# Kernel optimization log

Measured on AMD Instinct MI355X. Metric: run time of the kernel, lower is better.

Reference implementation:

```python
import jax, jax.numpy as jnp
import numpy as np

B, S, E, H = 2, 2048, 1024, 16
D = E // H  # head_dim = 64


def setup_inputs() -> dict:
    key = jax.random.key(0)
    ks = jax.random.split(key, 6)
    sc = 1.0 / np.sqrt(D)
    return {
        "x": jax.random.normal(ks[0], (B, S, E), dtype=jnp.float32),
        "Wq": jax.random.normal(ks[1], (D, D), dtype=jnp.float32) * sc,
        "Wk": jax.random.normal(ks[2], (D, D), dtype=jnp.float32) * sc,
        "Wv": jax.random.normal(ks[3], (D, D), dtype=jnp.float32) * sc,
        "Wo": jax.random.normal(ks[4], (E, E), dtype=jnp.float32) * (1.0 / np.sqrt(E)),
        "bo": jnp.zeros((E,), dtype=jnp.float32),
    }


def reference(x, Wq, Wk, Wv, Wo, bo):
    b, s, e = x.shape
    # split into heads: (B, H, S, D)
    xh = x.reshape(b, s, H, D).transpose(0, 2, 1, 3)
    # per-head linear projections (weights SHARED across heads); torch Linear: x @ W^T
    q = jnp.einsum('bhsd,ed->bhse', xh, Wq)
    k = jnp.einsum('bhsd,ed->bhse', xh, Wk)
    v = jnp.einsum('bhsd,ed->bhse', xh, Wv)
    # full attention matrix (B, H, S, S) — faithful to the naive original
    energy = jnp.einsum('bhqd,bhkd->bhqk', q, k)
    attn = jax.nn.softmax(energy / jnp.sqrt(jnp.asarray(D, x.dtype)), axis=-1)
    out = jnp.einsum('bhqk,bhkd->bhqd', attn, v)
    out = out.transpose(0, 2, 1, 3).reshape(b, s, e)
    return out @ Wo.T + bo
```

## Files before the change

### kernel.cpp

```cpp
#include <hip/hip_runtime.h>
#include <hip/hip_bf16.h>

#define B 2
#define S 2048
#define E 1024
#define H 16
#define D 64

typedef unsigned short ushort_t;
typedef __attribute__((ext_vector_type(8))) short bf16x8;
typedef __attribute__((ext_vector_type(4))) float f32x4;
typedef __attribute__((ext_vector_type(16))) float f32x16;

static __device__ __forceinline__ ushort_t f2bf(float f) {
    union { float f; unsigned u; } v; v.f = f;
    unsigned r = v.u + 0x7fffu + ((v.u >> 16) & 1u);
    return (ushort_t)(r >> 16);
}

#define MFMA(a, b, c)   __builtin_amdgcn_mfma_f32_16x16x32_bf16((a), (b), (c), 0, 0, 0)
#define MFMA32(a, b, c) __builtin_amdgcn_mfma_f32_32x32x16_bf16((a), (b), (c), 0, 0, 0)
#define PACKBF(hi, lo) __builtin_amdgcn_perm((hi), (lo), 0x07060302u)

__global__ __launch_bounds__(256) void cvt_w(
    const float* __restrict__ Wq, const float* __restrict__ Wk, const float* __restrict__ Wv,
    const float* __restrict__ Wo,
    ushort_t* __restrict__ wqb, ushort_t* __restrict__ wkb, ushort_t* __restrict__ wvb,
    ushort_t* __restrict__ wob)
{
    int gid = blockIdx.x, t = threadIdx.x;
    if (gid < 1024) {
        int i = gid * 1024 + t * 4;
        float4 f = *(const float4*)(Wo + i);
        ushort4 u; u.x = f2bf(f.x); u.y = f2bf(f.y); u.z = f2bf(f.z); u.w = f2bf(f.w);
        *(ushort4*)(wob + i) = u;
    } else {
        int idx = (gid - 1024) * 1024 + t * 4;
        int which = idx >> 12, off = idx & 4095;
        const float* src = (which == 0) ? Wq : (which == 1) ? Wk : Wv;
        ushort_t* dst    = (which == 0) ? wqb : (which == 1) ? wkb : wvb;
        float sc = (which == 0) ? 0.18033688011112042f : 1.0f;
        float4 f = *(const float4*)(src + off);
        ushort4 u; u.x = f2bf(f.x * sc); u.y = f2bf(f.y * sc);
        u.z = f2bf(f.z * sc); u.w = f2bf(f.w * sc);
        *(ushort4*)(dst + off) = u;
    }
}

__global__ __launch_bounds__(256) void qkv_proj(
    const float* __restrict__ x,
    const ushort_t* __restrict__ wq, const ushort_t* __restrict__ wk, const ushort_t* __restrict__ wv,
    ushort_t* __restrict__ q, ushort_t* __restrict__ k, ushort_t* __restrict__ vT)
{
    __shared__ ushort_t Xs[64][72];
    __shared__ ushort_t Wqs[64][72], Wks[64][72], Wvs[64][72];
    int t = threadIdx.x;
    int bh = blockIdx.y, b = bh >> 4, h = bh & 15;
    int s0 = blockIdx.x * 64;

    {
        int i = t >> 2, d0 = (t & 3) * 16;
        const float* xp = x + ((size_t)(b * S + s0 + i)) * E + h * D + d0;
        #pragma unroll
        for (int c = 0; c < 16; c += 4) {
            float4 f = *(const float4*)(xp + c);
            Xs[i][d0 + c + 0] = f2bf(f.x); Xs[i][d0 + c + 1] = f2bf(f.y);
            Xs[i][d0 + c + 2] = f2bf(f.z); Xs[i][d0 + c + 3] = f2bf(f.w);
        }
    }
    {
        int e = t >> 2, d0 = (t & 3) * 16;
        *(bf16x8*)&Wqs[e][d0]     = *(const bf16x8*)(wq + e * 64 + d0);
        *(bf16x8*)&Wqs[e][d0 + 8] = *(const bf16x8*)(wq + e * 64 + d0 + 8);
        *(bf16x8*)&Wks[e][d0]     = *(const bf16x8*)(wk + e * 64 + d0);
        *(bf16x8*)&Wks[e][d0 + 8] = *(const bf16x8*)(wk + e * 64 + d0 + 8);
        *(bf16x8*)&Wvs[e][d0]     = *(const bf16x8*)(wv + e * 64 + d0);
        *(bf16x8*)&Wvs[e][d0 + 8] = *(const bf16x8*)(wv + e * 64 + d0 + 8);
    }
    __syncthreads();

    int w = t >> 6, lane = t & 63, m = lane & 15, quad = lane >> 4;
    bf16x8 a0 = *(bf16x8*)&Xs[16 * w + m][quad * 8];
    bf16x8 a1 = *(bf16x8*)&Xs[16 * w + m][32 + quad * 8];
    f32x4 cq[4], ck[4], cv[4];
    #pragma unroll
    for (int nt = 0; nt < 4; nt++) { cq[nt] = (f32x4)0.f; ck[nt] = (f32x4)0.f; cv[nt] = (f32x4)0.f; }
    #pragma unroll
    for (int nt = 0; nt < 4; nt++) {
        bf16x8 b0, b1;
        b0 = *(bf16x8*)&Wqs[nt * 16 + m][quad * 8]; b1 = *(bf16x8*)&Wqs[nt * 16 + m][32 + quad * 8];
        cq[nt] = MFMA(a0, b0, cq[nt]); cq[nt] = MFMA(a1, b1, cq[nt]);
        b0 = *(bf16x8*)&Wks[nt * 16 + m][quad * 8]; b1 = *(bf16x8*)&Wks[nt * 16 + m][32 + quad * 8];
        ck[nt] = MFMA(a0, b0, ck[nt]); ck[nt] = MFMA(a1, b1, ck[nt]);
        b0 = *(bf16x8*)&Wvs[nt * 16 + m][quad * 8]; b1 = *(bf16x8*)&Wvs[nt * 16 + m][32 + quad * 8];
        cv[nt] = MFMA(a0, b0, cv[nt]); cv[nt] = MFMA(a1, b1, cv[nt]);
    }
    size_t base = (size_t)bh * S + s0;
    #pragma unroll
    for (int nt = 0; nt < 4; nt++)
        #pragma unroll
        for (int r = 0; r < 4; r++) {
            size_t idx = (base + 16 * w + quad * 4 + r) * D + nt * 16 + m;
            q[idx] = f2bf(cq[nt][r]);
            k[idx] = f2bf(ck[nt][r]);
        }
    __syncthreads();
    #pragma unroll
    for (int nt = 0; nt < 4; nt++)
        #pragma unroll
        for (int r = 0; r < 4; r++)
            Wvs[nt * 16 + m][16 * w + quad * 4 + r] = f2bf(cv[nt][r]);
    __syncthreads();
    {
        int d0 = t >> 2, sc = (t & 3) * 16;
        ushort_t* vp = vT + ((size_t)bh * D + d0) * S + s0 + sc;
        *(bf16x8*)(vp)     = *(bf16x8*)&Wvs[d0][sc];
        *(bf16x8*)(vp + 8) = *(bf16x8*)&Wvs[d0][sc + 8];
    }
}

__global__ __launch_bounds__(256) void flash_attn(
    const ushort_t* __restrict__ q, const ushort_t* __restrict__ k,
    const ushort_t* __restrict__ vT, ushort_t* __restrict__ ao)
{
    __shared__ ushort_t Ks[2][64][72];
    __shared__ ushort_t Vt[2][64][72];
    int t = threadIdx.x;
    int bh = blockIdx.y, b = bh >> 4, h = bh & 15;
    int q0 = blockIdx.x * 128;
    int w = t >> 6, lane = t & 63, l31 = lane & 31, half = lane >> 5;

    const ushort_t* qb = q + ((size_t)bh * S + q0) * D;
    const ushort_t* kb = k + (size_t)bh * S * D;
    const ushort_t* vb = vT + (size_t)bh * D * S;

    bf16x8 qf[4];
    {
        const ushort_t* qp = qb + (size_t)(w * 32 + l31) * D + half * 8;
        #pragma unroll
        for (int c = 0; c < 4; c++) qf[c] = *(const bf16x8*)(qp + c * 16);
    }

    f32x16 o0 = (f32x16)0.f, o1 = (f32x16)0.f;
    float2 ls2 = make_float2(0.f, 0.f);

    int sr = t >> 2, scc = (t & 3) * 16;
    bf16x8 kp0, kp1, vp0, vp1;

    {
        const ushort_t* kp = kb + (size_t)sr * D + scc;
        const ushort_t* vp = vb + (size_t)sr * S + scc;
        kp0 = *(const bf16x8*)(kp);     kp1 = *(const bf16x8*)(kp + 8);
        vp0 = *(const bf16x8*)(vp);     vp1 = *(const bf16x8*)(vp + 8);
        *(bf16x8*)&Ks[0][sr][scc]     = kp0;
        *(bf16x8*)&Ks[0][sr][scc + 8] = kp1;
        *(bf16x8*)&Vt[0][sr][scc]     = vp0;
        *(bf16x8*)&Vt[0][sr][scc + 8] = vp1;
    }
    __syncthreads();
    {
        const ushort_t* kp = kb + (size_t)(64 + sr) * D + scc;
        const ushort_t* vp = vb + (size_t)sr * S + 64 + scc;
        kp0 = *(const bf16x8*)(kp);     kp1 = *(const bf16x8*)(kp + 8);
        vp0 = *(const bf16x8*)(vp);     vp1 = *(const bf16x8*)(vp + 8);
    }

    const int NT = S / 64;
    for (int it = 0; it < NT; it++) {
        int p = it & 1;
        if (it + 1 < NT) {
            *(bf16x8*)&Ks[1 - p][sr][scc]     = kp0;
            *(bf16x8*)&Ks[1 - p][sr][scc + 8] = kp1;
            *(bf16x8*)&Vt[1 - p][sr][scc]     = vp0;
            *(bf16x8*)&Vt[1 - p][sr][scc + 8] = vp1;
        }
        if (it + 2 < NT) {
            int k0n = (it + 2) * 64;
            const ushort_t* kp = kb + (size_t)(k0n + sr) * D + scc;
            const ushort_t* vp = vb + (size_t)sr * S + k0n + scc;
            kp0 = *(const bf16x8*)(kp);     kp1 = *(const bf16x8*)(kp + 8);
            vp0 = *(const bf16x8*)(vp);     vp1 = *(const bf16x8*)(vp + 8);
        }

        union { unsigned u[4]; bf16x8 v; } pa[4];
        #pragma unroll
        for (int st = 0; st < 2; st++) {
            f32x16 e = (f32x16)0.f;
            #pragma unroll
            for (int c = 0; c < 4; c++) {
                bf16x8 ka = *(bf16x8*)&Ks[p][st * 32 + l31][c * 16 + half * 8];
                e = MFMA32(ka, qf[c], e);
            }
            unsigned pt[16];
            #pragma unroll
            for (int r = 0; r < 16; r += 2) {
                float pe0 = __builtin_amdgcn_exp2f(e[r]);
                float pe1 = __builtin_amdgcn_exp2f(e[r + 1]);
                ls2.x += pe0; ls2.y += pe1;
                pt[r]     = __float_as_uint(pe0);
                pt[r + 1] = __float_as_uint(pe1);
            }
            #pragma unroll
            for (int c2 = 0; c2 < 2; c2++) {
                int rb = c2 * 8;
                unsigned dA = PACKBF(pt[rb + 1], pt[rb + 0]);
                unsigned dB = PACKBF(pt[rb + 3], pt[rb + 2]);
                unsigned dC = PACKBF(pt[rb + 5], pt[rb + 4]);
                unsigned dD = PACKBF(pt[rb + 7], pt[rb + 6]);
                unsigned x1 = (unsigned)__shfl_xor((int)(half ? dA : dC), 32, 64);
                unsigned x2 = (unsigned)__shfl_xor((int)(half ? dB : dD), 32, 64);
                int kc = st * 2 + c2;
                pa[kc].u[0] = half ? x1 : dA;
                pa[kc].u[1] = half ? x2 : dB;
                pa[kc].u[2] = half ? dC : x1;
                pa[kc].u[3] = half ? dD : x2;
            }
        }

        #pragma unroll
        for (int kc = 0; kc < 4; kc++) {
            bf16x8 vf0 = *(bf16x8*)&Vt[p][l31][kc * 16 + half * 8];
            bf16x8 vf1 = *(bf16x8*)&Vt[p][32 + l31][kc * 16 + half * 8];
            o0 = MFMA32(pa[kc].v, vf0, o0);
            o1 = MFMA32(pa[kc].v, vf1, o1);
        }
        __syncthreads();
    }

    float lsum = ls2.x + ls2.y;
    float lfull = lsum + __shfl_xor(lsum, 32, 64);
    float inv = 1.001953125f / lfull;
    #pragma unroll
    for (int reg = 0; reg < 16; reg++) {
        int qrow = (reg & 3) + 8 * (reg >> 2) + 4 * half;
        float li = __shfl(inv, qrow, 64);
        int srow = q0 + w * 32 + qrow;
        size_t base = ((size_t)(b * S + srow)) * E + h * D + l31;
        ao[base]      = f2bf(o0[reg] * li);
        ao[base + 32] = f2bf(o1[reg] * li);
    }
}

__global__ __launch_bounds__(256) void out_proj(
    const ushort_t* __restrict__ A, const ushort_t* __restrict__ Wob,
    const float* __restrict__ bo, float* __restrict__ Y)
{
    __shared__ ushort_t As[2][128][72];
    __shared__ ushort_t Ws[2][64][72];
    int t = threadIdx.x;
    int n0 = blockIdx.x * 64, m0 = blockIdx.y * 128;
    int w = t >> 6, lane = t & 63, m = lane & 15, quad = lane >> 4;
    f32x4 acc[2][4];
    #pragma unroll
    for (int u = 0; u < 2; u++)
        #pragma unroll
        for (int nt = 0; nt < 4; nt++) acc[u][nt] = (f32x4)0.f;

    int ar = t >> 1, ac = (t & 1) * 32;
    int wr = t >> 2, wc = (t & 3) * 16;
    const ushort_t* apb = A + (size_t)(m0 + ar) * E + ac;
    const ushort_t* wpb = Wob + (size_t)(n0 + wr) * E + wc;

    bf16x8 arg[4], wrg[2];
    {
        #pragma unroll
        for (int i = 0; i < 4; i++) *(bf16x8*)&As[0][ar][ac + 8 * i] = *(const bf16x8*)(apb + 8 * i);
        *(bf16x8*)&Ws[0][wr][wc]     = *(const bf16x8*)(wpb);
        *(bf16x8*)&Ws[0][wr][wc + 8] = *(const bf16x8*)(wpb + 8);
    }
    __syncthreads();
    {
        #pragma unroll
        for (int i = 0; i < 4; i++) arg[i] = *(const bf16x8*)(apb + 64 + 8 * i);
        wrg[0] = *(const bf16x8*)(wpb + 64);
        wrg[1] = *(const bf16x8*)(wpb + 64 + 8);
    }

    const int KT = E / 64;
    for (int ks = 0; ks < KT; ks++) {
        int p = ks & 1;
        if (ks + 1 < KT) {
            #pragma unroll
            for (int i = 0; i < 4; i++) *(bf16x8*)&As[1 - p][ar][ac + 8 * i] = arg[i];
            *(bf16x8*)&Ws[1 - p][wr][wc]     = wrg[0];
            *(bf16x8*)&Ws[1 - p][wr][wc + 8] = wrg[1];
        }
        if (ks + 2 < KT) {
            int off = (ks + 2) * 64;
            #pragma unroll
            for (int i = 0; i < 4; i++) arg[i] = *(const bf16x8*)(apb + off + 8 * i);
            wrg[0] = *(const bf16x8*)(wpb + off);
            wrg[1] = *(const bf16x8*)(wpb + off + 8);
        }
        #pragma unroll
        for (int h2 = 0; h2 < 2; h2++) {
            bf16x8 af[2];
            af[0] = *(bf16x8*)&As[p][w * 32 + m][h2 * 32 + quad * 8];
            af[1] = *(bf16x8*)&As[p][w * 32 + 16 + m][h2 * 32 + quad * 8];
            #pragma unroll
            for (int nt = 0; nt < 4; nt++) {
                bf16x8 bfr = *(bf16x8*)&Ws[p][nt * 16 + m][h2 * 32 + quad * 8];
                acc[0][nt] = MFMA(af[0], bfr, acc[0][nt]);
                acc[1][nt] = MFMA(af[1], bfr, acc[1][nt]);
            }
        }
        __syncthreads();
    }
    #pragma unroll
    for (int u = 0; u < 2; u++)
        #pragma unroll
        for (int nt = 0; nt < 4; nt++)
            #pragma unroll
            for (int r = 0; r < 4; r++) {
                int row = m0 + w * 32 + u * 16 + quad * 4 + r;
                int col = n0 + nt * 16 + m;
                Y[(size_t)row * E + col] = acc[u][nt][r] + bo[col];
            }
}

extern "C" void kernel_launch(void* const* d_in, const int* in_sizes, int n_in,
                              void* d_out, int out_size, void* d_ws, size_t ws_size,
                              hipStream_t stream)
{
    const float* x  = (const float*)d_in[0];
    const float* Wq = (const float*)d_in[1];
    const float* Wk = (const float*)d_in[2];
    const float* Wv = (const float*)d_in[3];
    const float* Wo = (const float*)d_in[4];
    const float* bo = (const float*)d_in[5];
    float* Y = (float*)d_out;

    const size_t n = (size_t)B * H * S * D;
    ushort_t* qw  = (ushort_t*)d_ws;
    ushort_t* kw  = qw + n;
    ushort_t* vTw = kw + n;
    ushort_t* ao  = vTw + n;
    ushort_t* wob = ao + n;
    ushort_t* wqb = wob + (size_t)E * E;
    ushort_t* wkb = wqb + D * D;
    ushort_t* wvb = wkb + D * D;

    cvt_w<<<dim3(1024 + 12), 256, 0, stream>>>(Wq, Wk, Wv, Wo, wqb, wkb, wvb, wob);
    qkv_proj<<<dim3(S / 64, B * H), 256, 0, stream>>>(x, wqb, wkb, wvb, qw, kw, vTw);
    flash_attn<<<dim3(S / 128, B * H), 256, 0, stream>>>(qw, kw, vTw, ao);
    out_proj<<<dim3(E / 64, (B * S) / 128), 256, 0, stream>>>(ao, wob, bo, Y);
}
```

Baseline: 152.2 us.

## Fuse weight conversion into consumers and double per-warp query rows in attention

Drops the separate weight-conversion kernel: Q/K/V weights are now converted to bf16 inside qkv_proj, and Wo is converted on the fly inside out_proj's load pipeline. This removes one launch and a round trip of the converted weights through global memory. qkv_proj swaps MFMA operands so Q/K results can be stored as vectorized ushort4 rows instead of scalar stores. flash_attn moves to 128 threads with each warp handling two 32-row query groups, so each K fragment is reused twice. In exchange there are more registers per thread and fewer waves per block, and out_proj repeats the Wo fp32 conversion once per row tile.

```diff
diff --git a/kernel.cpp b/kernel.cpp
--- a/kernel.cpp
+++ b/kernel.cpp
@@ -18,38 +18,22 @@
     return (ushort_t)(r >> 16);
 }
 
+static __device__ __forceinline__ bf16x8 load_cvt8(const float* p) {
+    float4 f0 = *(const float4*)(p);
+    float4 f1 = *(const float4*)(p + 4);
+    union { ushort_t s[8]; bf16x8 v; } u;
+    u.s[0] = f2bf(f0.x); u.s[1] = f2bf(f0.y); u.s[2] = f2bf(f0.z); u.s[3] = f2bf(f0.w);
+    u.s[4] = f2bf(f1.x); u.s[5] = f2bf(f1.y); u.s[6] = f2bf(f1.z); u.s[7] = f2bf(f1.w);
+    return u.v;
+}
+
 #define MFMA(a, b, c)   __builtin_amdgcn_mfma_f32_16x16x32_bf16((a), (b), (c), 0, 0, 0)
 #define MFMA32(a, b, c) __builtin_amdgcn_mfma_f32_32x32x16_bf16((a), (b), (c), 0, 0, 0)
 #define PACKBF(hi, lo) __builtin_amdgcn_perm((hi), (lo), 0x07060302u)
 
-__global__ __launch_bounds__(256) void cvt_w(
-    const float* __restrict__ Wq, const float* __restrict__ Wk, const float* __restrict__ Wv,
-    const float* __restrict__ Wo,
-    ushort_t* __restrict__ wqb, ushort_t* __restrict__ wkb, ushort_t* __restrict__ wvb,
-    ushort_t* __restrict__ wob)
-{
-    int gid = blockIdx.x, t = threadIdx.x;
-    if (gid < 1024) {
-        int i = gid * 1024 + t * 4;
-        float4 f = *(const float4*)(Wo + i);
-        ushort4 u; u.x = f2bf(f.x); u.y = f2bf(f.y); u.z = f2bf(f.z); u.w = f2bf(f.w);
-        *(ushort4*)(wob + i) = u;
-    } else {
-        int idx = (gid - 1024) * 1024 + t * 4;
-        int which = idx >> 12, off = idx & 4095;
-        const float* src = (which == 0) ? Wq : (which == 1) ? Wk : Wv;
-        ushort_t* dst    = (which == 0) ? wqb : (which == 1) ? wkb : wvb;
-        float sc = (which == 0) ? 0.18033688011112042f : 1.0f;
-        float4 f = *(const float4*)(src + off);
-        ushort4 u; u.x = f2bf(f.x * sc); u.y = f2bf(f.y * sc);
-        u.z = f2bf(f.z * sc); u.w = f2bf(f.w * sc);
-        *(ushort4*)(dst + off) = u;
-    }
-}
-
 __global__ __launch_bounds__(256) void qkv_proj(
     const float* __restrict__ x,
-    const ushort_t* __restrict__ wq, const ushort_t* __restrict__ wk, const ushort_t* __restrict__ wv,
+    const float* __restrict__ Wq, const float* __restrict__ Wk, const float* __restrict__ Wv,
     ushort_t* __restrict__ q, ushort_t* __restrict__ k, ushort_t* __restrict__ vT)
 {
     __shared__ ushort_t Xs[64][72];
@@ -61,21 +45,30 @@
     {
         int i = t >> 2, d0 = (t & 3) * 16;
         const float* xp = x + ((size_t)(b * S + s0 + i)) * E + h * D + d0;
-        #pragma unroll
-        for (int c = 0; c < 16; c += 4) {
-            float4 f = *(const float4*)(xp + c);
-            Xs[i][d0 + c + 0] = f2bf(f.x); Xs[i][d0 + c + 1] = f2bf(f.y);
-            Xs[i][d0 + c + 2] = f2bf(f.z); Xs[i][d0 + c + 3] = f2bf(f.w);
-        }
+        *(bf16x8*)&Xs[i][d0]     = load_cvt8(xp);
+        *(bf16x8*)&Xs[i][d0 + 8] = load_cvt8(xp + 8);
     }
     {
         int e = t >> 2, d0 = (t & 3) * 16;
-        *(bf16x8*)&Wqs[e][d0]     = *(const bf16x8*)(wq + e * 64 + d0);
-        *(bf16x8*)&Wqs[e][d0 + 8] = *(const bf16x8*)(wq + e * 64 + d0 + 8);
-        *(bf16x8*)&Wks[e][d0]     = *(const bf16x8*)(wk + e * 64 + d0);
-        *(bf16x8*)&Wks[e][d0 + 8] = *(const bf16x8*)(wk + e * 64 + d0 + 8);
-        *(bf16x8*)&Wvs[e][d0]     = *(const bf16x8*)(wv + e * 64 + d0);
-        *(bf16x8*)&Wvs[e][d0 + 8] = *(const bf16x8*)(wv + e * 64 + d0 + 8);
+        const float* wqp = Wq + e * 64 + d0;
+        const float* wkp = Wk + e * 64 + d0;
+        const float* wvp = Wv + e * 64 + d0;
+        const float sc = 0.18033688011112042f;
+        {
+            float4 f0 = *(const float4*)(wqp), f1 = *(const float4*)(wqp + 4);
+            float4 f2 = *(const float4*)(wqp + 8), f3 = *(const float4*)(wqp + 12);
+            union { ushort_t s[16]; } u;
+            u.s[0]=f2bf(f0.x*sc); u.s[1]=f2bf(f0.y*sc); u.s[2]=f2bf(f0.z*sc); u.s[3]=f2bf(f0.w*sc);
+            u.s[4]=f2bf(f1.x*sc); u.s[5]=f2bf(f1.y*sc); u.s[6]=f2bf(f1.z*sc); u.s[7]=f2bf(f1.w*sc);
+            u.s[8]=f2bf(f2.x*sc); u.s[9]=f2bf(f2.y*sc); u.s[10]=f2bf(f2.z*sc); u.s[11]=f2bf(f2.w*sc);
+            u.s[12]=f2bf(f3.x*sc); u.s[13]=f2bf(f3.y*sc); u.s[14]=f2bf(f3.z*sc); u.s[15]=f2bf(f3.w*sc);
+            *(bf16x8*)&Wqs[e][d0]     = *(bf16x8*)&u.s[0];
+            *(bf16x8*)&Wqs[e][d0 + 8] = *(bf16x8*)&u.s[8];
+        }
+        *(bf16x8*)&Wks[e][d0]     = load_cvt8(wkp);
+        *(bf16x8*)&Wks[e][d0 + 8] = load_cvt8(wkp + 8);
+        *(bf16x8*)&Wvs[e][d0]     = load_cvt8(wvp);
+        *(bf16x8*)&Wvs[e][d0 + 8] = load_cvt8(wvp + 8);
     }
     __syncthreads();
 
@@ -89,27 +82,30 @@
     for (int nt = 0; nt < 4; nt++) {
         bf16x8 b0, b1;
         b0 = *(bf16x8*)&Wqs[nt * 16 + m][quad * 8]; b1 = *(bf16x8*)&Wqs[nt * 16 + m][32 + quad * 8];
-        cq[nt] = MFMA(a0, b0, cq[nt]); cq[nt] = MFMA(a1, b1, cq[nt]);
+        cq[nt] = MFMA(b0, a0, cq[nt]); cq[nt] = MFMA(b1, a1, cq[nt]);
         b0 = *(bf16x8*)&Wks[nt * 16 + m][quad * 8]; b1 = *(bf16x8*)&Wks[nt * 16 + m][32 + quad * 8];
-        ck[nt] = MFMA(a0, b0, ck[nt]); ck[nt] = MFMA(a1, b1, ck[nt]);
+        ck[nt] = MFMA(b0, a0, ck[nt]); ck[nt] = MFMA(b1, a1, ck[nt]);
         b0 = *(bf16x8*)&Wvs[nt * 16 + m][quad * 8]; b1 = *(bf16x8*)&Wvs[nt * 16 + m][32 + quad * 8];
-        cv[nt] = MFMA(a0, b0, cv[nt]); cv[nt] = MFMA(a1, b1, cv[nt]);
+        cv[nt] = MFMA(b0, a0, cv[nt]); cv[nt] = MFMA(b1, a1, cv[nt]);
     }
     size_t base = (size_t)bh * S + s0;
+    {
+        size_t rowoff = (base + 16 * w + m) * D + quad * 4;
+        #pragma unroll
+        for (int nt = 0; nt < 4; nt++) {
+            ushort4 uq, uk;
+            uq.x = f2bf(cq[nt][0]); uq.y = f2bf(cq[nt][1]); uq.z = f2bf(cq[nt][2]); uq.w = f2bf(cq[nt][3]);
+            uk.x = f2bf(ck[nt][0]); uk.y = f2bf(ck[nt][1]); uk.z = f2bf(ck[nt][2]); uk.w = f2bf(ck[nt][3]);
+            *(ushort4*)(q + rowoff + nt * 16) = uq;
+            *(ushort4*)(k + rowoff + nt * 16) = uk;
+        }
+    }
+    __syncthreads();
     #pragma unroll
     for (int nt = 0; nt < 4; nt++)
         #pragma unroll
-        for (int r = 0; r < 4; r++) {
-            size_t idx = (base + 16 * w + quad * 4 + r) * D + nt * 16 + m;
-            q[idx] = f2bf(cq[nt][r]);
-            k[idx] = f2bf(ck[nt][r]);
-        }
-    __syncthreads();
-    #pragma unroll
-    for (int nt = 0; nt < 4; nt++)
-        #pragma unroll
         for (int r = 0; r < 4; r++)
-            Wvs[nt * 16 + m][16 * w + quad * 4 + r] = f2bf(cv[nt][r]);
+            Wvs[nt * 16 + quad * 4 + r][16 * w + m] = f2bf(cv[nt][r]);
     __syncthreads();
     {
         int d0 = t >> 2, sc = (t & 3) * 16;
@@ -119,7 +115,7 @@
     }
 }
 
-__global__ __launch_bounds__(256) void flash_attn(
+__global__ __launch_bounds__(128) void flash_attn(
     const ushort_t* __restrict__ q, const ushort_t* __restrict__ k,
     const ushort_t* __restrict__ vT, ushort_t* __restrict__ ao)
 {
@@ -134,86 +130,99 @@
     const ushort_t* kb = k + (size_t)bh * S * D;
     const ushort_t* vb = vT + (size_t)bh * D * S;
 
-    bf16x8 qf[4];
-    {
-        const ushort_t* qp = qb + (size_t)(w * 32 + l31) * D + half * 8;
-        #pragma unroll
-        for (int c = 0; c < 4; c++) qf[c] = *(const bf16x8*)(qp + c * 16);
-    }
-
-    f32x16 o0 = (f32x16)0.f, o1 = (f32x16)0.f;
-    float2 ls2 = make_float2(0.f, 0.f);
-
-    int sr = t >> 2, scc = (t & 3) * 16;
-    bf16x8 kp0, kp1, vp0, vp1;
+    bf16x8 qf[2][4];
+    #pragma unroll
+    for (int g = 0; g < 2; g++) {
+        const ushort_t* qp = qb + (size_t)(w * 64 + g * 32 + l31) * D + half * 8;
+        #pragma unroll
+        for (int c = 0; c < 4; c++) qf[g][c] = *(const bf16x8*)(qp + c * 16);
+    }
+
+    f32x16 o_[2][2];
+    float2 ls2[2];
+    #pragma unroll
+    for (int g = 0; g < 2; g++) {
+        o_[g][0] = (f32x16)0.f; o_[g][1] = (f32x16)0.f;
+        ls2[g] = make_float2(0.f, 0.f);
+    }
+
+    int sr = t >> 1, scc = (t & 1) * 32;
+    bf16x8 kpre[4], vpre[4];
 
     {
         const ushort_t* kp = kb + (size_t)sr * D + scc;
         const ushort_t* vp = vb + (size_t)sr * S + scc;
-        kp0 = *(const bf16x8*)(kp);     kp1 = *(const bf16x8*)(kp + 8);
-        vp0 = *(const bf16x8*)(vp);     vp1 = *(const bf16x8*)(vp + 8);
-        *(bf16x8*)&Ks[0][sr][scc]     = kp0;
-        *(bf16x8*)&Ks[0][sr][scc + 8] = kp1;
-        *(bf16x8*)&Vt[0][sr][scc]     = vp0;
-        *(bf16x8*)&Vt[0][sr][scc + 8] = vp1;
+        #pragma unroll
+        for (int j = 0; j < 4; j++) { kpre[j] = *(const bf16x8*)(kp + 8 * j); vpre[j] = *(const bf16x8*)(vp + 8 * j); }
+        #pragma unroll
+        for (int j = 0; j < 4; j++) {
+            *(bf16x8*)&Ks[0][sr][scc + 8 * j] = kpre[j];
+            *(bf16x8*)&Vt[0][sr][scc + 8 * j] = vpre[j];
+        }
     }
     __syncthreads();
     {
         const ushort_t* kp = kb + (size_t)(64 + sr) * D + scc;
         const ushort_t* vp = vb + (size_t)sr * S + 64 + scc;
-        kp0 = *(const bf16x8*)(kp);     kp1 = *(const bf16x8*)(kp + 8);
-        vp0 = *(const bf16x8*)(vp);     vp1 = *(const bf16x8*)(vp + 8);
+        #pragma unroll
+        for (int j = 0; j < 4; j++) { kpre[j] = *(const bf16x8*)(kp + 8 * j); vpre[j] = *(const bf16x8*)(vp + 8 * j); }
     }
 
     const int NT = S / 64;
     for (int it = 0; it < NT; it++) {
         int p = it & 1;
         if (it + 1 < NT) {
-            *(bf16x8*)&Ks[1 - p][sr][scc]     = kp0;
-            *(bf16x8*)&Ks[1 - p][sr][scc + 8] = kp1;
-            *(bf16x8*)&Vt[1 - p][sr][scc]     = vp0;
-            *(bf16x8*)&Vt[1 - p][sr][scc + 8] = vp1;
+            #pragma unroll
+            for (int j = 0; j < 4; j++) {
+                *(bf16x8*)&Ks[1 - p][sr][scc + 8 * j] = kpre[j];
+                *(bf16x8*)&Vt[1 - p][sr][scc + 8 * j] = vpre[j];
+            }
         }
         if (it + 2 < NT) {
             int k0n = (it + 2) * 64;
             const ushort_t* kp = kb + (size_t)(k0n + sr) * D + scc;
             const ushort_t* vp = vb + (size_t)sr * S + k0n + scc;
-            kp0 = *(const bf16x8*)(kp);     kp1 = *(const bf16x8*)(kp + 8);
-            vp0 = *(const bf16x8*)(vp);     vp1 = *(const bf16x8*)(vp + 8);
-        }
-
-        union { unsigned u[4]; bf16x8 v; } pa[4];
+            #pragma unroll
+            for (int j = 0; j < 4; j++) { kpre[j] = *(const bf16x8*)(kp + 8 * j); vpre[j] = *(const bf16x8*)(vp + 8 * j); }
+        }
+
+        union { unsigned u[4]; bf16x8 v; } pa[2][4];
         #pragma unroll
         for (int st = 0; st < 2; st++) {
-            f32x16 e = (f32x16)0.f;
-            #pragma unroll
-            for (int c = 0; c < 4; c++) {
-                bf16x8 ka = *(bf16x8*)&Ks[p][st * 32 + l31][c * 16 + half * 8];
-                e = MFMA32(ka, qf[c], e);
-            }
-            unsigned pt[16];
-            #pragma unroll
-            for (int r = 0; r < 16; r += 2) {
-                float pe0 = __builtin_amdgcn_exp2f(e[r]);
-                float pe1 = __builtin_amdgcn_exp2f(e[r + 1]);
-                ls2.x += pe0; ls2.y += pe1;
-                pt[r]     = __float_as_uint(pe0);
-                pt[r + 1] = __float_as_uint(pe1);
-            }
-            #pragma unroll
-            for (int c2 = 0; c2 < 2; c2++) {
-                int rb = c2 * 8;
-                unsigned dA = PACKBF(pt[rb + 1], pt[rb + 0]);
-                unsigned dB = PACKBF(pt[rb + 3], pt[rb + 2]);
-                unsigned dC = PACKBF(pt[rb + 5], pt[rb + 4]);
-                unsigned dD = PACKBF(pt[rb + 7], pt[rb + 6]);
-                unsigned x1 = (unsigned)__shfl_xor((int)(half ? dA : dC), 32, 64);
-                unsigned x2 = (unsigned)__shfl_xor((int)(half ? dB : dD), 32, 64);
-                int kc = st * 2 + c2;
-                pa[kc].u[0] = half ? x1 : dA;
-                pa[kc].u[1] = half ? x2 : dB;
-                pa[kc].u[2] = half ? dC : x1;
-                pa[kc].u[3] = half ? dD : x2;
+            bf16x8 ka[4];
+            #pragma unroll
+            for (int c = 0; c < 4; c++)
+                ka[c] = *(bf16x8*)&Ks[p][st * 32 + l31][c * 16 + half * 8];
+            #pragma unroll
+            for (int g = 0; g < 2; g++) {
+                f32x16 e = (f32x16)0.f;
+                #pragma unroll
+                for (int c = 0; c < 4; c++)
+                    e = MFMA32(ka[c], qf[g][c], e);
+                unsigned pt[16];
+                #pragma unroll
+                for (int r = 0; r < 16; r += 2) {
+                    float pe0 = __builtin_amdgcn_exp2f(e[r]);
+                    float pe1 = __builtin_amdgcn_exp2f(e[r + 1]);
+                    ls2[g].x += pe0; ls2[g].y += pe1;
+                    pt[r]     = __float_as_uint(pe0);
+                    pt[r + 1] = __float_as_uint(pe1);
+                }
+                #pragma unroll
+                for (int c2 = 0; c2 < 2; c2++) {
+                    int rb = c2 * 8;
+                    unsigned dA = PACKBF(pt[rb + 1], pt[rb + 0]);
+                    unsigned dB = PACKBF(pt[rb + 3], pt[rb + 2]);
+                    unsigned dC = PACKBF(pt[rb + 5], pt[rb + 4]);
+                    unsigned dD = PACKBF(pt[rb + 7], pt[rb + 6]);
+                    unsigned x1 = (unsigned)__shfl_xor((int)(half ? dA : dC), 32, 64);
+                    unsigned x2 = (unsigned)__shfl_xor((int)(half ? dB : dD), 32, 64);
+                    int kc = st * 2 + c2;
+                    pa[g][kc].u[0] = half ? x1 : dA;
+                    pa[g][kc].u[1] = half ? x2 : dB;
+                    pa[g][kc].u[2] = half ? dC : x1;
+                    pa[g][kc].u[3] = half ? dD : x2;
+                }
             }
         }
 
@@ -221,28 +230,34 @@
         for (int kc = 0; kc < 4; kc++) {
             bf16x8 vf0 = *(bf16x8*)&Vt[p][l31][kc * 16 + half * 8];
             bf16x8 vf1 = *(bf16x8*)&Vt[p][32 + l31][kc * 16 + half * 8];
-            o0 = MFMA32(pa[kc].v, vf0, o0);
-            o1 = MFMA32(pa[kc].v, vf1, o1);
+            #pragma unroll
+            for (int g = 0; g < 2; g++) {
+                o_[g][0] = MFMA32(pa[g][kc].v, vf0, o_[g][0]);
+                o_[g][1] = MFMA32(pa[g][kc].v, vf1, o_[g][1]);
+            }
         }
         __syncthreads();
     }
 
-    float lsum = ls2.x + ls2.y;
-    float lfull = lsum + __shfl_xor(lsum, 32, 64);
-    float inv = 1.001953125f / lfull;
-    #pragma unroll
-    for (int reg = 0; reg < 16; reg++) {
-        int qrow = (reg & 3) + 8 * (reg >> 2) + 4 * half;
-        float li = __shfl(inv, qrow, 64);
-        int srow = q0 + w * 32 + qrow;
-        size_t base = ((size_t)(b * S + srow)) * E + h * D + l31;
-        ao[base]      = f2bf(o0[reg] * li);
-        ao[base + 32] = f2bf(o1[reg] * li);
+    #pragma unroll
+    for (int g = 0; g < 2; g++) {
+        float lsum = ls2[g].x + ls2[g].y;
+        float lfull = lsum + __shfl_xor(lsum, 32, 64);
+        float inv = 1.001953125f / lfull;
+        #pragma unroll
+        for (int reg = 0; reg < 16; reg++) {
+            int qrow = (reg & 3) + 8 * (reg >> 2) + 4 * half;
+            float li = __shfl(inv, qrow, 64);
+            int srow = q0 + w * 64 + g * 32 + qrow;
+            size_t base = ((size_t)(b * S + srow)) * E + h * D + l31;
+            ao[base]      = f2bf(o_[g][0][reg] * li);
+            ao[base + 32] = f2bf(o_[g][1][reg] * li);
+        }
     }
 }
 
 __global__ __launch_bounds__(256) void out_proj(
-    const ushort_t* __restrict__ A, const ushort_t* __restrict__ Wob,
+    const ushort_t* __restrict__ A, const float* __restrict__ Wo,
     const float* __restrict__ bo, float* __restrict__ Y)
 {
     __shared__ ushort_t As[2][128][72];
@@ -259,21 +274,21 @@
     int ar = t >> 1, ac = (t & 1) * 32;
     int wr = t >> 2, wc = (t & 3) * 16;
     const ushort_t* apb = A + (size_t)(m0 + ar) * E + ac;
-    const ushort_t* wpb = Wob + (size_t)(n0 + wr) * E + wc;
+    const float*    wpb = Wo + (size_t)(n0 + wr) * E + wc;
 
     bf16x8 arg[4], wrg[2];
     {
         #pragma unroll
         for (int i = 0; i < 4; i++) *(bf16x8*)&As[0][ar][ac + 8 * i] = *(const bf16x8*)(apb + 8 * i);
-        *(bf16x8*)&Ws[0][wr][wc]     = *(const bf16x8*)(wpb);
-        *(bf16x8*)&Ws[0][wr][wc + 8] = *(const bf16x8*)(wpb + 8);
+        *(bf16x8*)&Ws[0][wr][wc]     = load_cvt8(wpb);
+        *(bf16x8*)&Ws[0][wr][wc + 8] = load_cvt8(wpb + 8);
     }
     __syncthreads();
     {
         #pragma unroll
         for (int i = 0; i < 4; i++) arg[i] = *(const bf16x8*)(apb + 64 + 8 * i);
-        wrg[0] = *(const bf16x8*)(wpb + 64);
-        wrg[1] = *(const bf16x8*)(wpb + 64 + 8);
+        wrg[0] = load_cvt8(wpb + 64);
+        wrg[1] = load_cvt8(wpb + 64 + 8);
     }
 
     const int KT = E / 64;
@@ -289,8 +304,8 @@
             int off = (ks + 2) * 64;
             #pragma unroll
             for (int i = 0; i < 4; i++) arg[i] = *(const bf16x8*)(apb + off + 8 * i);
-            wrg[0] = *(const bf16x8*)(wpb + off);
-            wrg[1] = *(const bf16x8*)(wpb + off + 8);
+            wrg[0] = load_cvt8(wpb + off);
+            wrg[1] = load_cvt8(wpb + off + 8);
         }
         #pragma unroll
         for (int h2 = 0; h2 < 2; h2++) {
@@ -335,13 +350,8 @@
     ushort_t* kw  = qw + n;
     ushort_t* vTw = kw + n;
     ushort_t* ao  = vTw + n;
-    ushort_t* wob = ao + n;
-    ushort_t* wqb = wob + (size_t)E * E;
-    ushort_t* wkb = wqb + D * D;
-    ushort_t* wvb = wkb + D * D;
-
-    cvt_w<<<dim3(1024 + 12), 256, 0, stream>>>(Wq, Wk, Wv, Wo, wqb, wkb, wvb, wob);
-    qkv_proj<<<dim3(S / 64, B * H), 256, 0, stream>>>(x, wqb, wkb, wvb, qw, kw, vTw);
-    flash_attn<<<dim3(S / 128, B * H), 256, 0, stream>>>(qw, kw, vTw, ao);
-    out_proj<<<dim3(E / 64, (B * S) / 128), 256, 0, stream>>>(ao, wob, bo, Y);
-}
+
+    qkv_proj<<<dim3(S / 64, B * H), 256, 0, stream>>>(x, Wq, Wk, Wv, qw, kw, vTw);
+    flash_attn<<<dim3(S / 128, B * H), 128, 0, stream>>>(qw, kw, vTw, ao);
+    out_proj<<<dim3(E / 64, (B * S) / 128), 256, 0, stream>>>(ao, Wo, bo, Y);
+}
```

Result: slower. 160.1 us (+5.2%).
